# Optimization experiments

Hardware: AMD Instinct MI355X
Metric: run time of the kernel (lower is better)

## Reference

```python
import jax, jax.numpy as jnp
import numpy as np

L, D, DH, NH, P = 12, 768, 64, 12, 16
B, H_IMG, W_IMG = 16, 384, 384
MAX_GRID = 64


def setup_inputs() -> dict:
    key = jax.random.key(0)
    ks = jax.random.split(key, 10)
    r = lambda k, shp: (0.02 * jax.random.normal(k, shp, dtype=jnp.float32))
    return {
        "x": jax.random.normal(ks[0], (B, 3, H_IMG, W_IMG), dtype=jnp.float32),
        "conv_w": r(ks[1], (D, 3, P, P)),
        "conv_b": jnp.zeros((D,), jnp.float32),
        "ln_w": jnp.ones((D,), jnp.float32),
        "ln_b": jnp.zeros((D,), jnp.float32),
        "pos_y_emb": r(ks[2], (MAX_GRID, D)),
        "pos_x_emb": r(ks[3], (MAX_GRID, D)),
        "mha_ln_w": jnp.ones((L, D), jnp.float32),
        "mha_ln_b": jnp.zeros((L, D), jnp.float32),
        "qw": r(ks[4], (L, D, D)),
        "kw": r(ks[5], (L, D, D)),
        "vw": r(ks[6], (L, D, D)),
        "ffn_ln_w": jnp.ones((L, D), jnp.float32),
        "ffn_ln_b": jnp.zeros((L, D), jnp.float32),
        "w1": r(ks[7], (L, D, 4 * D)),
        "b1": jnp.zeros((L, 4 * D), jnp.float32),
        "w2": r(ks[8], (L, 4 * D, D)),
        "b2": jnp.zeros((L, D), jnp.float32),
        "x_shift": 0,
        "y_shift": 0,
    }


def _ln(x, w, b):
    m = jnp.mean(x, axis=-1, keepdims=True)
    v = jnp.var(x, axis=-1, keepdims=True)
    return (x - m) * jax.lax.rsqrt(v + 1e-5) * w + b


def reference(x, conv_w, conv_b, ln_w, ln_b, pos_y_emb, pos_x_emb,
              mha_ln_w, mha_ln_b, qw, kw, vw,
              ffn_ln_w, ffn_ln_b, w1, b1, w2, b2, x_shift, y_shift):
    # patch embed: conv + relu, to NHWC, layernorm
    h = jax.lax.conv_general_dilated(x, conv_w, (P, P), 'VALID',
                                     dimension_numbers=('NCHW', 'OIHW', 'NCHW'))
    h = jax.nn.relu(h + conv_b[None, :, None, None])
    h = jnp.transpose(h, (0, 2, 3, 1))  # [B, GH, GW, D]
    h = _ln(h, ln_w, ln_b)
    b, gh, gw, d = h.shape
    n = gh * gw
    # 2D factorized positional embedding, shared layernorm
    pos = (pos_y_emb[jnp.arange(gh) + y_shift][:, None, :]
           + pos_x_emb[jnp.arange(gw) + x_shift][None, :, :])  # [GH, GW, D]
    pos = _ln(pos, ln_w, ln_b).reshape(1, n, d)
    pos_emb = jnp.broadcast_to(pos, (b, n, d))
    t = h.reshape(b, n, d) + pos_emb
    scale = 1.0 / jnp.sqrt(jnp.float32(DH))
    for i in range(L):
        # pre-LN MHA (no output projection, mask=None / pretrain=False)
        tl = _ln(t, mha_ln_w[i], mha_ln_b[i])
        q = (tl @ qw[i]).reshape(b, n, NH, DH).transpose(0, 2, 1, 3)
        k = (tl @ kw[i]).reshape(b, n, NH, DH).transpose(0, 2, 1, 3)
        v = (tl @ vw[i]).reshape(b, n, NH, DH).transpose(0, 2, 1, 3)
        attn = jax.nn.softmax(jnp.einsum('bhqd,bhkd->bhqk', q, k) * scale, axis=-1)
        o = jnp.einsum('bhqk,bhkd->bhqd', attn, v).transpose(0, 2, 1, 3).reshape(b, n, d)
        t = t + o
        fl = _ln(t, ffn_ln_w[i], ffn_ln_b[i])
        t = t + (jax.nn.relu(fl @ w1[i] + b1[i]) @ w2[i] + b2[i])
    return t, pos_emb
```

## Files before the change

kernel.cpp:

```cpp
#include <hip/hip_runtime.h>

typedef unsigned short u16;
typedef __attribute__((ext_vector_type(4))) float f32x4;
typedef __attribute__((ext_vector_type(8))) short s16x8;

__device__ __forceinline__ u16 f2bf(float f) {
    union { float f; unsigned u; } v; v.f = f;
    unsigned r = v.u + 0x7FFFu + ((v.u >> 16) & 1u);
    return (u16)(r >> 16);
}

__device__ __forceinline__ void gload_lds16(const u16* g, u16* l) {
    __builtin_amdgcn_global_load_lds(
        (const __attribute__((address_space(1))) unsigned int*)(g),
        (__attribute__((address_space(3))) unsigned int*)(l),
        16, 0, 0);
}

#define NTOK 9216
#define SEQ  576
#define DMODEL 768
#define DFF  3072
#define NHEAD 12
#define HDIM 64

__global__ __launch_bounds__(256) void convert_bf16_kernel(const float* __restrict__ in,
                                                           u16* __restrict__ out, int n) {
    for (int i = blockIdx.x * 256 + threadIdx.x; i < n; i += gridDim.x * 256)
        out[i] = f2bf(in[i]);
}

__global__ __launch_bounds__(256) void copy_f32_kernel(const float* __restrict__ in,
                                                       float* __restrict__ out, int n4) {
    const float4* a = (const float4*)in;
    float4* o = (float4*)out;
    for (int i = blockIdx.x * 256 + threadIdx.x; i < n4; i += gridDim.x * 256)
        o[i] = a[i];
}

__global__ __launch_bounds__(256) void im2col_kernel(const float* __restrict__ x,
                                                     u16* __restrict__ out) {
    int tok = blockIdx.x;
    int b = tok / SEQ, n = tok % SEQ;
    int gy = n / 24, gx = n % 24;
    int tid = threadIdx.x;
#pragma unroll
    for (int j = 0; j < 3; ++j) {
        int col = tid + j * 256;
        int c = col >> 8, py = (col >> 4) & 15, px = col & 15;
        float v = x[(size_t)((b * 3 + c) * 384 + gy * 16 + py) * 384 + gx * 16 + px];
        out[(size_t)tok * DMODEL + col] = f2bf(v);
    }
}

__global__ __launch_bounds__(256) void transpose_layer_kernel(
        const float* __restrict__ qw, const float* __restrict__ kw, const float* __restrict__ vw,
        const float* __restrict__ w1, const float* __restrict__ w2,
        u16* __restrict__ wTq, u16* __restrict__ wTk, u16* __restrict__ wTv,
        u16* __restrict__ w1T, u16* __restrict__ w2T) {
    int bid = blockIdx.x;
    const float* src; u16* dst; int Kd, Nd, tile;
    if (bid < 1728)      { int m = bid / 576; src = m == 0 ? qw : (m == 1 ? kw : vw);
                           dst = m == 0 ? wTq : (m == 1 ? wTk : wTv); Kd = 768; Nd = 768; tile = bid % 576; }
    else if (bid < 4032) { src = w1; dst = w1T; Kd = 768; Nd = 3072; tile = bid - 1728; }
    else                 { src = w2; dst = w2T; Kd = 3072; Nd = 768; tile = bid - 4032; }
    int ntx = Nd / 32;
    int tk = (tile / ntx) * 32, tn = (tile % ntx) * 32;
    __shared__ float ts[32][33];
    int tx = threadIdx.x & 31, ty = threadIdx.x >> 5;
#pragma unroll
    for (int j = 0; j < 32; j += 8)
        ts[ty + j][tx] = src[(size_t)(tk + ty + j) * Nd + tn + tx];
    __syncthreads();
#pragma unroll
    for (int j = 0; j < 32; j += 8)
        dst[(size_t)(tn + ty + j) * Kd + tk + tx] = f2bf(ts[tx][ty + j]);
}

__global__ __launch_bounds__(256) void ln_bf16_kernel(const float* __restrict__ X,
                                                      const float* __restrict__ w,
                                                      const float* __restrict__ b,
                                                      u16* __restrict__ Y) {
    int row = blockIdx.x, tid = threadIdx.x;
    const float* x = X + (size_t)row * DMODEL;
    float v0 = x[tid], v1 = x[tid + 256], v2 = x[tid + 512];
    float s = v0 + v1 + v2, sq = v0 * v0 + v1 * v1 + v2 * v2;
#pragma unroll
    for (int off = 32; off >= 1; off >>= 1) { s += __shfl_down(s, off); sq += __shfl_down(sq, off); }
    __shared__ float red[8];
    if ((tid & 63) == 0) { red[tid >> 6] = s; red[4 + (tid >> 6)] = sq; }
    __syncthreads();
    float S = red[0] + red[1] + red[2] + red[3];
    float Q = red[4] + red[5] + red[6] + red[7];
    float mean = S * (1.f / DMODEL);
    float var = Q * (1.f / DMODEL) - mean * mean;
    float inv = rsqrtf(var + 1e-5f);
    u16* y = Y + (size_t)row * DMODEL;
    y[tid]       = f2bf((v0 - mean) * inv * w[tid]       + b[tid]);
    y[tid + 256] = f2bf((v1 - mean) * inv * w[tid + 256] + b[tid + 256]);
    y[tid + 512] = f2bf((v2 - mean) * inv * w[tid + 512] + b[tid + 512]);
}

__global__ __launch_bounds__(256) void ln_add_pos_kernel(float* __restrict__ T,
                                                         const float* __restrict__ w,
                                                         const float* __restrict__ b,
                                                         const float* __restrict__ posln) {
    int row = blockIdx.x, tid = threadIdx.x;
    float* x = T + (size_t)row * DMODEL;
    const float* p = posln + (size_t)(row % SEQ) * DMODEL;
    float v0 = x[tid], v1 = x[tid + 256], v2 = x[tid + 512];
    float s = v0 + v1 + v2, sq = v0 * v0 + v1 * v1 + v2 * v2;
#pragma unroll
    for (int off = 32; off >= 1; off >>= 1) { s += __shfl_down(s, off); sq += __shfl_down(sq, off); }
    __shared__ float red[8];
    if ((tid & 63) == 0) { red[tid >> 6] = s; red[4 + (tid >> 6)] = sq; }
    __syncthreads();
    float S = red[0] + red[1] + red[2] + red[3];
    float Q = red[4] + red[5] + red[6] + red[7];
    float mean = S * (1.f / DMODEL);
    float var = Q * (1.f / DMODEL) - mean * mean;
    float inv = rsqrtf(var + 1e-5f);
    x[tid]       = (v0 - mean) * inv * w[tid]       + b[tid]       + p[tid];
    x[tid + 256] = (v1 - mean) * inv * w[tid + 256] + b[tid + 256] + p[tid + 256];
    x[tid + 512] = (v2 - mean) * inv * w[tid + 512] + b[tid + 512] + p[tid + 512];
}

__global__ __launch_bounds__(256) void pos_ln_kernel(const float* __restrict__ py,
                                                     const float* __restrict__ px,
                                                     const float* __restrict__ w,
                                                     const float* __restrict__ b,
                                                     const int* __restrict__ xs_p,
                                                     const int* __restrict__ ys_p,
                                                     float* __restrict__ posln,
                                                     float* __restrict__ out2) {
    int row = blockIdx.x;
    int gy = row / 24, gx = row % 24;
    int ys = ys_p[0], xs = xs_p[0];
    int tid = threadIdx.x;
    float v[3]; float s = 0.f, sq = 0.f;
#pragma unroll
    for (int j = 0; j < 3; ++j) {
        int c = tid + j * 256;
        v[j] = py[(size_t)(gy + ys) * DMODEL + c] + px[(size_t)(gx + xs) * DMODEL + c];
        s += v[j]; sq += v[j] * v[j];
    }
#pragma unroll
    for (int off = 32; off >= 1; off >>= 1) { s += __shfl_down(s, off); sq += __shfl_down(sq, off); }
    __shared__ float red[8];
    if ((tid & 63) == 0) { red[tid >> 6] = s; red[4 + (tid >> 6)] = sq; }
    __syncthreads();
    float S = red[0] + red[1] + red[2] + red[3];
    float Q = red[4] + red[5] + red[6] + red[7];
    float mean = S * (1.f / DMODEL);
    float var = Q * (1.f / DMODEL) - mean * mean;
    float inv = rsqrtf(var + 1e-5f);
#pragma unroll
    for (int j = 0; j < 3; ++j) {
        int c = tid + j * 256;
        float y = (v[j] - mean) * inv * w[c] + b[c];
        posln[(size_t)row * DMODEL + c] = y;
        for (int bb = 0; bb < 16; ++bb)
            out2[((size_t)bb * SEQ + row) * DMODEL + c] = y;
    }
}

#define EPI_CONV 0
#define EPI_QKV  1
#define EPI_FFN1 3
#define EPI_FFN2 4

template <int EPI>
__global__ __launch_bounds__(512, 2) void gemm3(const u16* __restrict__ A,
                                                const u16* __restrict__ Bt,
                                                float* __restrict__ outF,
                                                u16* __restrict__ outB,
                                                u16* __restrict__ outB2,
                                                u16* __restrict__ outB3,
                                                const float* __restrict__ bias,
                                                int M, int N, int K) {
    __shared__ __align__(16) u16 lds[3 * 24576];
    const int tid = threadIdx.x;
    const int wave = tid >> 6, lane = tid & 63;
    const int c_lo = lane & 15, c_hi = lane >> 4;
    const int wm = wave >> 2, wn = wave & 3;
    const int m0 = blockIdx.x * 128, n0 = blockIdx.y * 256;

    int rowA[2], kkA[2], rowB[4], kkB[4];
#pragma unroll
    for (int r = 0; r < 2; ++r) {
        int L = r * 8192 + tid * 16;
        int P = L ^ ((L >> 3) & 0x70);
        rowA[r] = P >> 7; kkA[r] = (P & 127) >> 1;
    }
#pragma unroll
    for (int r = 0; r < 4; ++r) {
        int L = r * 8192 + tid * 16;
        int P = L ^ ((L >> 3) & 0x70);
        rowB[r] = P >> 7; kkB[r] = (P & 127) >> 1;
    }
    const int NT = K >> 6;
    f32x4 acc[4][4] = {};

    auto stage = [&](int t) {
        u16* buf = lds + (t % 3) * 24576;
        int k0 = t << 6;
#pragma unroll
        for (int r = 0; r < 2; ++r)
            gload_lds16(A + (size_t)(m0 + rowA[r]) * K + k0 + kkA[r],
                        buf + r * 4096 + wave * 512);
#pragma unroll
        for (int r = 0; r < 4; ++r)
            gload_lds16(Bt + (size_t)(n0 + rowB[r]) * K + k0 + kkB[r],
                        buf + 8192 + r * 4096 + wave * 512);
    };

    stage(0); stage(1);
    asm volatile("s_waitcnt vmcnt(6)" ::: "memory");
    __builtin_amdgcn_s_barrier();
    __builtin_amdgcn_sched_barrier(0);

    for (int t = 0; t < NT; ++t) {
        if (t + 2 < NT) stage(t + 2);
        const u16* Ab = lds + (t % 3) * 24576;
        const u16* Bb = Ab + 8192;
        s16x8 af[4][2], bf[4][2];
#pragma unroll
        for (int mf = 0; mf < 4; ++mf)
#pragma unroll
            for (int ks = 0; ks < 2; ++ks) {
                int by = (wm * 64 + mf * 16 + c_lo) * 128 + (ks * 32 + c_hi * 8) * 2;
                by ^= (by >> 3) & 0x70;
                af[mf][ks] = *(const s16x8*)((const char*)Ab + by);
            }
#pragma unroll
        for (int nf = 0; nf < 4; ++nf)
#pragma unroll
            for (int ks = 0; ks < 2; ++ks) {
                int by = (wn * 64 + nf * 16 + c_lo) * 128 + (ks * 32 + c_hi * 8) * 2;
                by ^= (by >> 3) & 0x70;
                bf[nf][ks] = *(const s16x8*)((const char*)Bb + by);
            }
        __builtin_amdgcn_s_setprio(1);
#pragma unroll
        for (int mf = 0; mf < 4; ++mf)
#pragma unroll
            for (int nf = 0; nf < 4; ++nf)
#pragma unroll
                for (int ks = 0; ks < 2; ++ks)
                    acc[mf][nf] = __builtin_amdgcn_mfma_f32_16x16x32_bf16(
                        af[mf][ks], bf[nf][ks], acc[mf][nf], 0, 0, 0);
        __builtin_amdgcn_s_setprio(0);
        if (t + 2 < NT) { asm volatile("s_waitcnt vmcnt(6)" ::: "memory"); }
        else            { asm volatile("s_waitcnt vmcnt(0)" ::: "memory"); }
        __builtin_amdgcn_s_barrier();
        __builtin_amdgcn_sched_barrier(0);
    }

#pragma unroll
    for (int mf = 0; mf < 4; ++mf)
#pragma unroll
        for (int nf = 0; nf < 4; ++nf)
#pragma unroll
            for (int r = 0; r < 4; ++r) {
                int grow = m0 + wm * 64 + mf * 16 + c_hi * 4 + r;
                int gcol = n0 + wn * 64 + nf * 16 + c_lo;
                float v = acc[mf][nf][r];
                if (EPI == EPI_CONV) {
                    v += bias[gcol]; v = fmaxf(v, 0.f);
                    outF[(size_t)grow * N + gcol] = v;
                } else if (EPI == EPI_QKV) {
                    int sel = n0 / 768;
                    int lcol = gcol - sel * 768;
                    if (sel == 0)      outB [(size_t)grow * 768 + lcol] = f2bf(v);
                    else if (sel == 1) outB2[(size_t)grow * 768 + lcol] = f2bf(v);
                    else {
                        int b = grow / SEQ, nt = grow % SEQ;
                        int h = lcol >> 6, dh = lcol & 63;
                        outB3[(size_t)(((b * NHEAD + h) << 6) + dh) * SEQ + nt] = f2bf(v);
                    }
                } else if (EPI == EPI_FFN1) {
                    v += bias[gcol]; v = fmaxf(v, 0.f);
                    outB[(size_t)grow * N + gcol] = f2bf(v);
                } else if (EPI == EPI_FFN2) {
                    outF[(size_t)grow * DMODEL + gcol] += v + bias[gcol];
                }
            }
}

__global__ __launch_bounds__(256) void attn_kernel(const u16* __restrict__ Qb,
                                                   const u16* __restrict__ Kb,
                                                   const u16* __restrict__ Vt,
                                                   float* __restrict__ T) {
    int bid = blockIdx.x;
    int qt = bid % 9, h = (bid / 9) % NHEAD, b = bid / (9 * NHEAD);
    int q0 = qt * 64;
    const int tid = threadIdx.x, wave = tid >> 6, lane = tid & 63;
    const int c_lo = lane & 15, c_hi = lane >> 4;
    __shared__ __align__(16) u16 Qs[64][72];
    __shared__ __align__(16) u16 Ks[64][72];
    __shared__ __align__(16) u16 Vs[64][72];
    __shared__ __align__(16) u16 Ps[4][16][72];
#pragma unroll
    for (int i = 0; i < 2; ++i) {
        int c = i * 256 + tid, row = c >> 3, slot = (c & 7) * 8;
        *(s16x8*)&Qs[row][slot] =
            *(const s16x8*)(Qb + ((size_t)(b * SEQ + q0 + row) * DMODEL + h * HDIM + slot));
    }
    f32x4 o[4] = {};
    float mrun[4], lrun[4];
#pragma unroll
    for (int r = 0; r < 4; ++r) { mrun[r] = -1e30f; lrun[r] = 0.f; }
    for (int t2 = 0; t2 < 9; ++t2) {
        int kv0 = t2 * 64;
        __syncthreads();
#pragma unroll
        for (int i = 0; i < 2; ++i) {
            int c = i * 256 + tid, row = c >> 3, slot = (c & 7) * 8;
            *(s16x8*)&Ks[row][slot] =
                *(const s16x8*)(Kb + ((size_t)(b * SEQ + kv0 + row) * DMODEL + h * HDIM + slot));
            *(s16x8*)&Vs[row][slot] =
                *(const s16x8*)(Vt + ((size_t)((b * NHEAD + h) * HDIM + row) * SEQ + kv0 + slot));
        }
        __syncthreads();
        f32x4 s[4] = {};
        s16x8 aq[2];
#pragma unroll
        for (int ks = 0; ks < 2; ++ks)
            aq[ks] = *(const s16x8*)&Qs[wave * 16 + c_lo][ks * 32 + c_hi * 8];
#pragma unroll
        for (int nf = 0; nf < 4; ++nf)
#pragma unroll
            for (int ks = 0; ks < 2; ++ks) {
                s16x8 bk = *(const s16x8*)&Ks[nf * 16 + c_lo][ks * 32 + c_hi * 8];
                s[nf] = __builtin_amdgcn_mfma_f32_16x16x32_bf16(aq[ks], bk, s[nf], 0, 0, 0);
            }
#pragma unroll
        for (int nf = 0; nf < 4; ++nf)
#pragma unroll
            for (int r = 0; r < 4; ++r) s[nf][r] *= 0.125f;
        float mx[4];
#pragma unroll
        for (int r = 0; r < 4; ++r)
            mx[r] = fmaxf(fmaxf(s[0][r], s[1][r]), fmaxf(s[2][r], s[3][r]));
#pragma unroll
        for (int off = 1; off < 16; off <<= 1)
#pragma unroll
            for (int r = 0; r < 4; ++r) mx[r] = fmaxf(mx[r], __shfl_xor(mx[r], off));
        float alpha[4];
#pragma unroll
        for (int r = 0; r < 4; ++r) {
            float mn = fmaxf(mrun[r], mx[r]);
            alpha[r] = __expf(mrun[r] - mn);
            mrun[r] = mn;
            lrun[r] *= alpha[r];
        }
        float ls[4] = {0.f, 0.f, 0.f, 0.f};
        u16 pb[4][4];
#pragma unroll
        for (int nf = 0; nf < 4; ++nf)
#pragma unroll
            for (int r = 0; r < 4; ++r) {
                float p = __expf(s[nf][r] - mrun[r]);
                ls[r] += p;
                pb[nf][r] = f2bf(p);
            }
#pragma unroll
        for (int off = 1; off < 16; off <<= 1)
#pragma unroll
            for (int r = 0; r < 4; ++r) ls[r] += __shfl_xor(ls[r], off);
#pragma unroll
        for (int r = 0; r < 4; ++r) lrun[r] += ls[r];
#pragma unroll
        for (int df = 0; df < 4; ++df)
#pragma unroll
            for (int r = 0; r < 4; ++r) o[df][r] *= alpha[r];
#pragma unroll
        for (int nf = 0; nf < 4; ++nf)
#pragma unroll
            for (int r = 0; r < 4; ++r)
                Ps[wave][c_hi * 4 + r][c_lo + nf * 16] = pb[nf][r];
        asm volatile("s_waitcnt lgkmcnt(0)" ::: "memory");
        s16x8 pa[2];
#pragma unroll
        for (int ks = 0; ks < 2; ++ks)
            pa[ks] = *(const s16x8*)&Ps[wave][c_lo][ks * 32 + c_hi * 8];
#pragma unroll
        for (int df = 0; df < 4; ++df)
#pragma unroll
            for (int ks = 0; ks < 2; ++ks) {
                s16x8 bv = *(const s16x8*)&Vs[df * 16 + c_lo][ks * 32 + c_hi * 8];
                o[df] = __builtin_amdgcn_mfma_f32_16x16x32_bf16(pa[ks], bv, o[df], 0, 0, 0);
            }
    }
#pragma unroll
    for (int df = 0; df < 4; ++df)
#pragma unroll
        for (int r = 0; r < 4; ++r) {
            int grow = b * SEQ + q0 + wave * 16 + c_hi * 4 + r;
            int gcol = h * HDIM + df * 16 + c_lo;
            T[(size_t)grow * DMODEL + gcol] += o[df][r] / lrun[r];
        }
}

extern "C" void kernel_launch(void* const* d_in, const int* in_sizes, int n_in,
                              void* d_out, int out_size, void* d_ws, size_t ws_size,
                              hipStream_t stream) {
    (void)in_sizes; (void)n_in; (void)out_size; (void)ws_size;
    const float* x        = (const float*)d_in[0];
    const float* conv_w   = (const float*)d_in[1];
    const float* conv_b   = (const float*)d_in[2];
    const float* ln_w     = (const float*)d_in[3];
    const float* ln_b     = (const float*)d_in[4];
    const float* pos_y    = (const float*)d_in[5];
    const float* pos_x    = (const float*)d_in[6];
    const float* mha_ln_w = (const float*)d_in[7];
    const float* mha_ln_b = (const float*)d_in[8];
    const float* qw       = (const float*)d_in[9];
    const float* kw       = (const float*)d_in[10];
    const float* vw       = (const float*)d_in[11];
    const float* ffn_ln_w = (const float*)d_in[12];
    const float* ffn_ln_b = (const float*)d_in[13];
    const float* w1       = (const float*)d_in[14];
    const float* b1       = (const float*)d_in[15];
    const float* w2       = (const float*)d_in[16];
    const float* b2       = (const float*)d_in[17];
    const int*   xs       = (const int*)d_in[18];
    const int*   ys       = (const int*)d_in[19];
    float* out1 = (float*)d_out;
    float* out2 = out1 + (size_t)NTOK * DMODEL;

    size_t off = 0;
    char* ws = (char*)d_ws;
    auto carve = [&](size_t bytes) { char* p = ws + off; off += (bytes + 255) & ~(size_t)255; return p; };
    u16* wTqkv = (u16*)carve((size_t)3 * 768 * 768 * 2);
    u16* w1T = (u16*)carve((size_t)DFF * DMODEL * 2);
    u16* w2T = (u16*)carve((size_t)DMODEL * DFF * 2);
    float* t  = (float*)carve((size_t)NTOK * DMODEL * 4);
    u16* tl   = (u16*)carve((size_t)NTOK * DMODEL * 2);
    u16* qb   = (u16*)carve((size_t)NTOK * DMODEL * 2);
    u16* kb   = (u16*)carve((size_t)NTOK * DMODEL * 2);
    u16* vT   = (u16*)carve((size_t)NTOK * DMODEL * 2);
    u16* hb   = (u16*)carve((size_t)NTOK * DFF * 2);
    float* posln = (float*)carve((size_t)SEQ * DMODEL * 4);
    u16* wTq = wTqkv;
    u16* wTk = wTqkv + (size_t)768 * 768;
    u16* wTv = wTqkv + (size_t)2 * 768 * 768;
    u16* cw   = wTqkv;
    u16* im2c = hb;

    convert_bf16_kernel<<<1152, 256, 0, stream>>>(conv_w, cw, 768 * 768);
    im2col_kernel<<<NTOK, 256, 0, stream>>>(x, im2c);
    gemm3<EPI_CONV><<<dim3(72, 3), 512, 0, stream>>>(im2c, cw, t, nullptr, nullptr, nullptr,
                                                     conv_b, NTOK, DMODEL, DMODEL);
    pos_ln_kernel<<<SEQ, 256, 0, stream>>>(pos_y, pos_x, ln_w, ln_b, xs, ys, posln, out2);
    ln_add_pos_kernel<<<NTOK, 256, 0, stream>>>(t, ln_w, ln_b, posln);

    for (int i = 0; i < 12; ++i) {
        transpose_layer_kernel<<<6336, 256, 0, stream>>>(
            qw + (size_t)i * 768 * 768, kw + (size_t)i * 768 * 768, vw + (size_t)i * 768 * 768,
            w1 + (size_t)i * 768 * DFF, w2 + (size_t)i * DFF * 768,
            wTq, wTk, wTv, w1T, w2T);
        ln_bf16_kernel<<<NTOK, 256, 0, stream>>>(t, mha_ln_w + i * DMODEL, mha_ln_b + i * DMODEL, tl);
        gemm3<EPI_QKV><<<dim3(72, 9), 512, 0, stream>>>(tl, wTqkv, nullptr, qb, kb, vT,
                                                        nullptr, NTOK, 3 * DMODEL, DMODEL);
        attn_kernel<<<16 * NHEAD * 9, 256, 0, stream>>>(qb, kb, vT, t);
        ln_bf16_kernel<<<NTOK, 256, 0, stream>>>(t, ffn_ln_w + i * DMODEL, ffn_ln_b + i * DMODEL, tl);
        gemm3<EPI_FFN1><<<dim3(72, 12), 512, 0, stream>>>(tl, w1T, nullptr, hb, nullptr, nullptr,
                                                          b1 + (size_t)i * DFF, NTOK, DFF, DMODEL);
        gemm3<EPI_FFN2><<<dim3(72, 3), 512, 0, stream>>>(hb, w2T, t, nullptr, nullptr, nullptr,
                                                         b2 + (size_t)i * DMODEL, NTOK, DMODEL, DFF);
    }
    copy_f32_kernel<<<2048, 256, 0, stream>>>(t, out1, (NTOK * DMODEL) / 4);
}
```

Before: 3.256 ms.

## Use 256x256 double-buffered GEMM for QKV/FFN1 and register-prefetch K/V in attention

```diff
diff --git a/kernel.cpp b/kernel.cpp
--- a/kernel.cpp
+++ b/kernel.cpp
@@ -170,7 +170,7 @@
 #define EPI_FFN2 4
 
 template <int EPI>
-__global__ __launch_bounds__(512, 2) void gemm3(const u16* __restrict__ A,
+__global__ __launch_bounds__(512, 2) void gemm8(const u16* __restrict__ A,
                                                 const u16* __restrict__ Bt,
                                                 float* __restrict__ outF,
                                                 u16* __restrict__ outB,
@@ -178,97 +178,96 @@
                                                 u16* __restrict__ outB3,
                                                 const float* __restrict__ bias,
                                                 int M, int N, int K) {
-    __shared__ __align__(16) u16 lds[3 * 24576];
+    __shared__ __align__(16) u16 lds[2 * 32768];
     const int tid = threadIdx.x;
     const int wave = tid >> 6, lane = tid & 63;
     const int c_lo = lane & 15, c_hi = lane >> 4;
     const int wm = wave >> 2, wn = wave & 3;
-    const int m0 = blockIdx.x * 128, n0 = blockIdx.y * 256;
-
-    int rowA[2], kkA[2], rowB[4], kkB[4];
-#pragma unroll
-    for (int r = 0; r < 2; ++r) {
-        int L = r * 8192 + tid * 16;
-        int P = L ^ ((L >> 3) & 0x70);
-        rowA[r] = P >> 7; kkA[r] = (P & 127) >> 1;
-    }
+    const int m0 = blockIdx.x * 256, n0 = blockIdx.y * 256;
+
+    const u16* srcA[4]; const u16* srcB[4]; int dA[4], dB[4];
 #pragma unroll
     for (int r = 0; r < 4; ++r) {
         int L = r * 8192 + tid * 16;
         int P = L ^ ((L >> 3) & 0x70);
-        rowB[r] = P >> 7; kkB[r] = (P & 127) >> 1;
+        srcA[r] = A  + (size_t)(m0 + (P >> 7)) * K + ((P & 127) >> 1);
+        srcB[r] = Bt + (size_t)(n0 + (P >> 7)) * K + ((P & 127) >> 1);
+        dA[r] = r * 4096 + tid * 8;
+        dB[r] = 16384 + r * 4096 + tid * 8;
     }
     const int NT = K >> 6;
-    f32x4 acc[4][4] = {};
+    f32x4 acc[8][4] = {};
 
     auto stage = [&](int t) {
-        u16* buf = lds + (t % 3) * 24576;
-        int k0 = t << 6;
-#pragma unroll
-        for (int r = 0; r < 2; ++r)
-            gload_lds16(A + (size_t)(m0 + rowA[r]) * K + k0 + kkA[r],
-                        buf + r * 4096 + wave * 512);
-#pragma unroll
-        for (int r = 0; r < 4; ++r)
-            gload_lds16(Bt + (size_t)(n0 + rowB[r]) * K + k0 + kkB[r],
-                        buf + 8192 + r * 4096 + wave * 512);
+        u16* buf = lds + (t & 1) * 32768;
+        int ko = t << 6;
+#pragma unroll
+        for (int r = 0; r < 4; ++r) {
+            gload_lds16(srcA[r] + ko, buf + dA[r]);
+            gload_lds16(srcB[r] + ko, buf + dB[r]);
+        }
     };
 
-    stage(0); stage(1);
-    asm volatile("s_waitcnt vmcnt(6)" ::: "memory");
+    stage(0);
+    asm volatile("s_waitcnt vmcnt(0)" ::: "memory");
     __builtin_amdgcn_s_barrier();
     __builtin_amdgcn_sched_barrier(0);
 
     for (int t = 0; t < NT; ++t) {
-        if (t + 2 < NT) stage(t + 2);
-        const u16* Ab = lds + (t % 3) * 24576;
-        const u16* Bb = Ab + 8192;
-        s16x8 af[4][2], bf[4][2];
-#pragma unroll
-        for (int mf = 0; mf < 4; ++mf)
-#pragma unroll
-            for (int ks = 0; ks < 2; ++ks) {
-                int by = (wm * 64 + mf * 16 + c_lo) * 128 + (ks * 32 + c_hi * 8) * 2;
-                by ^= (by >> 3) & 0x70;
-                af[mf][ks] = *(const s16x8*)((const char*)Ab + by);
-            }
-#pragma unroll
-        for (int nf = 0; nf < 4; ++nf)
-#pragma unroll
-            for (int ks = 0; ks < 2; ++ks) {
-                int by = (wn * 64 + nf * 16 + c_lo) * 128 + (ks * 32 + c_hi * 8) * 2;
-                by ^= (by >> 3) & 0x70;
-                bf[nf][ks] = *(const s16x8*)((const char*)Bb + by);
-            }
-        __builtin_amdgcn_s_setprio(1);
-#pragma unroll
-        for (int mf = 0; mf < 4; ++mf)
-#pragma unroll
-            for (int nf = 0; nf < 4; ++nf)
-#pragma unroll
-                for (int ks = 0; ks < 2; ++ks)
-                    acc[mf][nf] = __builtin_amdgcn_mfma_f32_16x16x32_bf16(
-                        af[mf][ks], bf[nf][ks], acc[mf][nf], 0, 0, 0);
-        __builtin_amdgcn_s_setprio(0);
-        if (t + 2 < NT) { asm volatile("s_waitcnt vmcnt(6)" ::: "memory"); }
-        else            { asm volatile("s_waitcnt vmcnt(0)" ::: "memory"); }
-        __builtin_amdgcn_s_barrier();
+        if (t + 1 < NT) stage(t + 1);
         __builtin_amdgcn_sched_barrier(0);
-    }
-
-#pragma unroll
-    for (int mf = 0; mf < 4; ++mf)
+        const char* Ab = (const char*)(lds + (t & 1) * 32768);
+        const char* Bb = Ab + 32768;
+#pragma unroll
+        for (int p = 0; p < 4; ++p) {
+            const int mh = p >> 1, nh = p & 1;
+            s16x8 af[4][2], bf[2][2];
+#pragma unroll
+            for (int i = 0; i < 4; ++i)
+#pragma unroll
+                for (int ks = 0; ks < 2; ++ks) {
+                    int by = (wm * 128 + (mh * 4 + i) * 16 + c_lo) * 128 + (ks * 32 + c_hi * 8) * 2;
+                    by ^= (by >> 3) & 0x70;
+                    af[i][ks] = *(const s16x8*)(Ab + by);
+                }
+#pragma unroll
+            for (int j = 0; j < 2; ++j)
+#pragma unroll
+                for (int ks = 0; ks < 2; ++ks) {
+                    int by = (wn * 64 + (nh * 2 + j) * 16 + c_lo) * 128 + (ks * 32 + c_hi * 8) * 2;
+                    by ^= (by >> 3) & 0x70;
+                    bf[j][ks] = *(const s16x8*)(Bb + by);
+                }
+            asm volatile("s_waitcnt lgkmcnt(0)" ::: "memory");
+            __builtin_amdgcn_sched_barrier(0);
+            __builtin_amdgcn_s_setprio(1);
+#pragma unroll
+            for (int i = 0; i < 4; ++i)
+#pragma unroll
+                for (int j = 0; j < 2; ++j)
+#pragma unroll
+                    for (int ks = 0; ks < 2; ++ks)
+                        acc[mh * 4 + i][nh * 2 + j] = __builtin_amdgcn_mfma_f32_16x16x32_bf16(
+                            af[i][ks], bf[j][ks], acc[mh * 4 + i][nh * 2 + j], 0, 0, 0);
+            __builtin_amdgcn_s_setprio(0);
+        }
+        if (t + 1 < NT) {
+            asm volatile("s_waitcnt vmcnt(0)" ::: "memory");
+            __builtin_amdgcn_s_barrier();
+            __builtin_amdgcn_sched_barrier(0);
+        }
+    }
+
+#pragma unroll
+    for (int mf = 0; mf < 8; ++mf)
 #pragma unroll
         for (int nf = 0; nf < 4; ++nf)
 #pragma unroll
             for (int r = 0; r < 4; ++r) {
-                int grow = m0 + wm * 64 + mf * 16 + c_hi * 4 + r;
+                int grow = m0 + wm * 128 + mf * 16 + c_hi * 4 + r;
                 int gcol = n0 + wn * 64 + nf * 16 + c_lo;
                 float v = acc[mf][nf][r];
-                if (EPI == EPI_CONV) {
-                    v += bias[gcol]; v = fmaxf(v, 0.f);
-                    outF[(size_t)grow * N + gcol] = v;
-                } else if (EPI == EPI_QKV) {
+                if (EPI == EPI_QKV) {
                     int sel = n0 / 768;
                     int lcol = gcol - sel * 768;
                     if (sel == 0)      outB [(size_t)grow * 768 + lcol] = f2bf(v);
@@ -281,6 +280,109 @@
                 } else if (EPI == EPI_FFN1) {
                     v += bias[gcol]; v = fmaxf(v, 0.f);
                     outB[(size_t)grow * N + gcol] = f2bf(v);
+                }
+            }
+}
+
+template <int EPI>
+__global__ __launch_bounds__(512, 2) void gemm3(const u16* __restrict__ A,
+                                                const u16* __restrict__ Bt,
+                                                float* __restrict__ outF,
+                                                u16* __restrict__ outB,
+                                                const float* __restrict__ bias,
+                                                int M, int N, int K) {
+    __shared__ __align__(16) u16 lds[3 * 24576];
+    const int tid = threadIdx.x;
+    const int wave = tid >> 6, lane = tid & 63;
+    const int c_lo = lane & 15, c_hi = lane >> 4;
+    const int wm = wave >> 2, wn = wave & 3;
+    const int m0 = blockIdx.x * 128, n0 = blockIdx.y * 256;
+
+    int rowA[2], kkA[2], rowB[4], kkB[4];
+#pragma unroll
+    for (int r = 0; r < 2; ++r) {
+        int L = r * 8192 + tid * 16;
+        int P = L ^ ((L >> 3) & 0x70);
+        rowA[r] = P >> 7; kkA[r] = (P & 127) >> 1;
+    }
+#pragma unroll
+    for (int r = 0; r < 4; ++r) {
+        int L = r * 8192 + tid * 16;
+        int P = L ^ ((L >> 3) & 0x70);
+        rowB[r] = P >> 7; kkB[r] = (P & 127) >> 1;
+    }
+    const int NT = K >> 6;
+    f32x4 acc[4][4] = {};
+
+    auto stage = [&](int t) {
+        u16* buf = lds + (t % 3) * 24576;
+        int k0 = t << 6;
+#pragma unroll
+        for (int r = 0; r < 2; ++r)
+            gload_lds16(A + (size_t)(m0 + rowA[r]) * K + k0 + kkA[r],
+                        buf + r * 4096 + wave * 512);
+#pragma unroll
+        for (int r = 0; r < 4; ++r)
+            gload_lds16(Bt + (size_t)(n0 + rowB[r]) * K + k0 + kkB[r],
+                        buf + 8192 + r * 4096 + wave * 512);
+    };
+
+    stage(0); stage(1);
+    asm volatile("s_waitcnt vmcnt(6)" ::: "memory");
+    __builtin_amdgcn_s_barrier();
+    __builtin_amdgcn_sched_barrier(0);
+
+    for (int t = 0; t < NT; ++t) {
+        if (t + 2 < NT) stage(t + 2);
+        const u16* Ab = lds + (t % 3) * 24576;
+        const u16* Bb = Ab + 8192;
+        s16x8 af[4][2], bf[4][2];
+#pragma unroll
+        for (int mf = 0; mf < 4; ++mf)
+#pragma unroll
+            for (int ks = 0; ks < 2; ++ks) {
+                int by = (wm * 64 + mf * 16 + c_lo) * 128 + (ks * 32 + c_hi * 8) * 2;
+                by ^= (by >> 3) & 0x70;
+                af[mf][ks] = *(const s16x8*)((const char*)Ab + by);
+            }
+#pragma unroll
+        for (int nf = 0; nf < 4; ++nf)
+#pragma unroll
+            for (int ks = 0; ks < 2; ++ks) {
+                int by = (wn * 64 + nf * 16 + c_lo) * 128 + (ks * 32 + c_hi * 8) * 2;
+                by ^= (by >> 3) & 0x70;
+                bf[nf][ks] = *(const s16x8*)((const char*)Bb + by);
+            }
+        asm volatile("s_waitcnt lgkmcnt(0)" ::: "memory");
+        __builtin_amdgcn_sched_barrier(0);
+        __builtin_amdgcn_s_setprio(1);
+#pragma unroll
+        for (int mf = 0; mf < 4; ++mf)
+#pragma unroll
+            for (int nf = 0; nf < 4; ++nf)
+#pragma unroll
+                for (int ks = 0; ks < 2; ++ks)
+                    acc[mf][nf] = __builtin_amdgcn_mfma_f32_16x16x32_bf16(
+                        af[mf][ks], bf[nf][ks], acc[mf][nf], 0, 0, 0);
+        __builtin_amdgcn_s_setprio(0);
+        if (t + 2 < NT) { asm volatile("s_waitcnt vmcnt(6)" ::: "memory"); }
+        else            { asm volatile("s_waitcnt vmcnt(0)" ::: "memory"); }
+        __builtin_amdgcn_s_barrier();
+        __builtin_amdgcn_sched_barrier(0);
+    }
+
+#pragma unroll
+    for (int mf = 0; mf < 4; ++mf)
+#pragma unroll
+        for (int nf = 0; nf < 4; ++nf)
+#pragma unroll
+            for (int r = 0; r < 4; ++r) {
+                int grow = m0 + wm * 64 + mf * 16 + c_hi * 4 + r;
+                int gcol = n0 + wn * 64 + nf * 16 + c_lo;
+                float v = acc[mf][nf][r];
+                if (EPI == EPI_CONV) {
+                    v += bias[gcol]; v = fmaxf(v, 0.f);
+                    outF[(size_t)grow * N + gcol] = v;
                 } else if (EPI == EPI_FFN2) {
                     outF[(size_t)grow * DMODEL + gcol] += v + bias[gcol];
                 }
@@ -292,7 +394,8 @@
                                                    const u16* __restrict__ Vt,
                                                    float* __restrict__ T) {
     int bid = blockIdx.x;
-    int qt = bid % 9, h = (bid / 9) % NHEAD, b = bid / (9 * NHEAD);
+    int qt = bid / 192, bh = bid % 192;
+    int b = bh / NHEAD, h = bh % NHEAD;
     int q0 = qt * 64;
     const int tid = threadIdx.x, wave = tid >> 6, lane = tid & 63;
     const int c_lo = lane & 15, c_hi = lane >> 4;
@@ -306,22 +409,39 @@
         *(s16x8*)&Qs[row][slot] =
             *(const s16x8*)(Qb + ((size_t)(b * SEQ + q0 + row) * DMODEL + h * HDIM + slot));
     }
+    s16x8 kreg[2], vreg[2];
+    {
+#pragma unroll
+        for (int i = 0; i < 2; ++i) {
+            int c = i * 256 + tid, row = c >> 3, slot = (c & 7) * 8;
+            kreg[i] = *(const s16x8*)(Kb + ((size_t)(b * SEQ + row) * DMODEL + h * HDIM + slot));
+            vreg[i] = *(const s16x8*)(Vt + ((size_t)((b * NHEAD + h) * HDIM + row) * SEQ + slot));
+        }
+    }
     f32x4 o[4] = {};
     float mrun[4], lrun[4];
 #pragma unroll
     for (int r = 0; r < 4; ++r) { mrun[r] = -1e30f; lrun[r] = 0.f; }
     for (int t2 = 0; t2 < 9; ++t2) {
-        int kv0 = t2 * 64;
-        __syncthreads();
+        __builtin_amdgcn_s_barrier();
 #pragma unroll
         for (int i = 0; i < 2; ++i) {
             int c = i * 256 + tid, row = c >> 3, slot = (c & 7) * 8;
-            *(s16x8*)&Ks[row][slot] =
-                *(const s16x8*)(Kb + ((size_t)(b * SEQ + kv0 + row) * DMODEL + h * HDIM + slot));
-            *(s16x8*)&Vs[row][slot] =
-                *(const s16x8*)(Vt + ((size_t)((b * NHEAD + h) * HDIM + row) * SEQ + kv0 + slot));
-        }
-        __syncthreads();
+            *(s16x8*)&Ks[row][slot] = kreg[i];
+            *(s16x8*)&Vs[row][slot] = vreg[i];
+        }
+        asm volatile("s_waitcnt lgkmcnt(0)" ::: "memory");
+        __builtin_amdgcn_s_barrier();
+        __builtin_amdgcn_sched_barrier(0);
+        if (t2 < 8) {
+            int kv0 = (t2 + 1) * 64;
+#pragma unroll
+            for (int i = 0; i < 2; ++i) {
+                int c = i * 256 + tid, row = c >> 3, slot = (c & 7) * 8;
+                kreg[i] = *(const s16x8*)(Kb + ((size_t)(b * SEQ + kv0 + row) * DMODEL + h * HDIM + slot));
+                vreg[i] = *(const s16x8*)(Vt + ((size_t)((b * NHEAD + h) * HDIM + row) * SEQ + kv0 + slot));
+            }
+        }
         f32x4 s[4] = {};
         s16x8 aq[2];
 #pragma unroll
@@ -450,7 +570,7 @@
 
     convert_bf16_kernel<<<1152, 256, 0, stream>>>(conv_w, cw, 768 * 768);
     im2col_kernel<<<NTOK, 256, 0, stream>>>(x, im2c);
-    gemm3<EPI_CONV><<<dim3(72, 3), 512, 0, stream>>>(im2c, cw, t, nullptr, nullptr, nullptr,
+    gemm3<EPI_CONV><<<dim3(72, 3), 512, 0, stream>>>(im2c, cw, t, nullptr,
                                                      conv_b, NTOK, DMODEL, DMODEL);
     pos_ln_kernel<<<SEQ, 256, 0, stream>>>(pos_y, pos_x, ln_w, ln_b, xs, ys, posln, out2);
     ln_add_pos_kernel<<<NTOK, 256, 0, stream>>>(t, ln_w, ln_b, posln);
@@ -461,13 +581,13 @@
             w1 + (size_t)i * 768 * DFF, w2 + (size_t)i * DFF * 768,
             wTq, wTk, wTv, w1T, w2T);
         ln_bf16_kernel<<<NTOK, 256, 0, stream>>>(t, mha_ln_w + i * DMODEL, mha_ln_b + i * DMODEL, tl);
-        gemm3<EPI_QKV><<<dim3(72, 9), 512, 0, stream>>>(tl, wTqkv, nullptr, qb, kb, vT,
+        gemm8<EPI_QKV><<<dim3(36, 9), 512, 0, stream>>>(tl, wTqkv, nullptr, qb, kb, vT,
                                                         nullptr, NTOK, 3 * DMODEL, DMODEL);
         attn_kernel<<<16 * NHEAD * 9, 256, 0, stream>>>(qb, kb, vT, t);
         ln_bf16_kernel<<<NTOK, 256, 0, stream>>>(t, ffn_ln_w + i * DMODEL, ffn_ln_b + i * DMODEL, tl);
-        gemm3<EPI_FFN1><<<dim3(72, 12), 512, 0, stream>>>(tl, w1T, nullptr, hb, nullptr, nullptr,
+        gemm8<EPI_FFN1><<<dim3(36, 12), 512, 0, stream>>>(tl, w1T, nullptr, hb, nullptr, nullptr,
                                                           b1 + (size_t)i * DFF, NTOK, DFF, DMODEL);
-        gemm3<EPI_FFN2><<<dim3(72, 3), 512, 0, stream>>>(hb, w2T, t, nullptr, nullptr, nullptr,
+        gemm3<EPI_FFN2><<<dim3(72, 3), 512, 0, stream>>>(hb, w2T, t, nullptr,
                                                          b2 + (size_t)i * DMODEL, NTOK, DMODEL, DFF);
     }
     copy_f32_kernel<<<2048, 256, 0, stream>>>(t, out1, (NTOK * DMODEL) / 4);
```

Result: slower. 3.403 ms (+4.5%).

## Replace GEMM with 256x256 tiles, XCD-aware remap, split-K FFN2 and prefetched attention

Applied to the files above, without the earlier changes.

```diff
diff --git a/kernel.cpp b/kernel.cpp
--- a/kernel.cpp
+++ b/kernel.cpp
@@ -169,105 +169,110 @@
 #define EPI_FFN1 3
 #define EPI_FFN2 4
 
-template <int EPI>
-__global__ __launch_bounds__(512, 2) void gemm3(const u16* __restrict__ A,
-                                                const u16* __restrict__ Bt,
-                                                float* __restrict__ outF,
-                                                u16* __restrict__ outB,
-                                                u16* __restrict__ outB2,
-                                                u16* __restrict__ outB3,
-                                                const float* __restrict__ bias,
-                                                int M, int N, int K) {
-    __shared__ __align__(16) u16 lds[3 * 24576];
+template <int EPI, int NKT>
+__global__ __launch_bounds__(512, 2) void gemm256(const u16* __restrict__ A,
+                                                  const u16* __restrict__ Bt,
+                                                  float* __restrict__ outF,
+                                                  u16* __restrict__ outB,
+                                                  u16* __restrict__ outB2,
+                                                  u16* __restrict__ outB3,
+                                                  const float* __restrict__ bias,
+                                                  int lda, int N, int NBY) {
+    __shared__ __align__(16) u16 lds[4 * 16384];
     const int tid = threadIdx.x;
     const int wave = tid >> 6, lane = tid & 63;
     const int c_lo = lane & 15, c_hi = lane >> 4;
     const int wm = wave >> 2, wn = wave & 3;
-    const int m0 = blockIdx.x * 128, n0 = blockIdx.y * 256;
-
-    int rowA[2], kkA[2], rowB[4], kkB[4];
-#pragma unroll
-    for (int r = 0; r < 2; ++r) {
-        int L = r * 8192 + tid * 16;
-        int P = L ^ ((L >> 3) & 0x70);
-        rowA[r] = P >> 7; kkA[r] = (P & 127) >> 1;
-    }
-#pragma unroll
-    for (int r = 0; r < 4; ++r) {
-        int L = r * 8192 + tid * 16;
-        int P = L ^ ((L >> 3) & 0x70);
-        rowB[r] = P >> 7; kkB[r] = (P & 127) >> 1;
-    }
-    const int NT = K >> 6;
-    f32x4 acc[4][4] = {};
-
-    auto stage = [&](int t) {
-        u16* buf = lds + (t % 3) * 24576;
-        int k0 = t << 6;
-#pragma unroll
-        for (int r = 0; r < 2; ++r)
-            gload_lds16(A + (size_t)(m0 + rowA[r]) * K + k0 + kkA[r],
-                        buf + r * 4096 + wave * 512);
-#pragma unroll
-        for (int r = 0; r < 4; ++r)
-            gload_lds16(Bt + (size_t)(n0 + rowB[r]) * K + k0 + kkB[r],
-                        buf + 8192 + r * 4096 + wave * 512);
+    int nwg = gridDim.x, bid = blockIdx.x;
+    int xcd = bid & 7, loc = bid >> 3;
+    int q = nwg >> 3, r = nwg & 7;
+    int lid = (xcd < r ? xcd * (q + 1) : r * (q + 1) + (xcd - r) * q) + loc;
+    int bx = lid % 36, rest = lid / 36;
+    int by = rest % NBY, bz = rest / NBY;
+    const int m0 = bx * 256, n0 = by * 256;
+    const int kb = bz * NKT * 32;
+
+    const u16* sA = A  + (size_t)(m0 + (tid >> 2)) * lda + kb + (tid & 3) * 8;
+    const u16* sB = Bt + (size_t)(n0 + (tid >> 2)) * lda + kb + (tid & 3) * 8;
+    const size_t rstep = (size_t)128 * lda;
+    f32x4 acc[8][4] = {};
+
+    auto stageA = [&](int kt) {
+        u16* d = lds + (kt & 3) * 16384 + tid * 8;
+        gload_lds16(sA + kt * 32, d);
+        gload_lds16(sA + rstep + kt * 32, d + 4096);
     };
-
-    stage(0); stage(1);
-    asm volatile("s_waitcnt vmcnt(6)" ::: "memory");
+    auto stageB = [&](int kt) {
+        u16* d = lds + (kt & 3) * 16384 + 8192 + tid * 8;
+        gload_lds16(sB + kt * 32, d);
+        gload_lds16(sB + rstep + kt * 32, d + 4096);
+    };
+
+    stageA(0); stageB(0); stageA(1); stageB(1); stageA(2); stageB(2);
+    asm volatile("s_waitcnt vmcnt(8)" ::: "memory");
     __builtin_amdgcn_s_barrier();
     __builtin_amdgcn_sched_barrier(0);
 
-    for (int t = 0; t < NT; ++t) {
-        if (t + 2 < NT) stage(t + 2);
-        const u16* Ab = lds + (t % 3) * 24576;
-        const u16* Bb = Ab + 8192;
-        s16x8 af[4][2], bf[4][2];
-#pragma unroll
-        for (int mf = 0; mf < 4; ++mf)
-#pragma unroll
-            for (int ks = 0; ks < 2; ++ks) {
-                int by = (wm * 64 + mf * 16 + c_lo) * 128 + (ks * 32 + c_hi * 8) * 2;
-                by ^= (by >> 3) & 0x70;
-                af[mf][ks] = *(const s16x8*)((const char*)Ab + by);
-            }
+    for (int j = 0; j < NKT; ++j) {
+        const u16* buf = lds + (j & 3) * 16384;
+        const bool st = (j + 3 < NKT);
+        s16x8 af[4], bf[4];
+#pragma unroll
+        for (int i = 0; i < 4; ++i) {
+            int row = wm * 128 + i * 16 + c_lo;
+            af[i] = *(const s16x8*)(buf + row * 32 + c_hi * 8);
+        }
+#pragma unroll
+        for (int n = 0; n < 4; ++n) {
+            int row = wn * 64 + n * 16 + c_lo;
+            bf[n] = *(const s16x8*)(buf + 8192 + row * 32 + c_hi * 8);
+        }
+        if (st) stageA(j + 3);
+        __builtin_amdgcn_s_barrier();
+        asm volatile("s_waitcnt lgkmcnt(0)" ::: "memory");
+        __builtin_amdgcn_sched_barrier(0);
+        __builtin_amdgcn_s_setprio(1);
+#pragma unroll
+        for (int i = 0; i < 4; ++i)
+#pragma unroll
+            for (int n = 0; n < 4; ++n)
+                acc[i][n] = __builtin_amdgcn_mfma_f32_16x16x32_bf16(af[i], bf[n], acc[i][n], 0, 0, 0);
+        __builtin_amdgcn_s_setprio(0);
+        __builtin_amdgcn_s_barrier();
+#pragma unroll
+        for (int i = 0; i < 4; ++i) {
+            int row = wm * 128 + 64 + i * 16 + c_lo;
+            af[i] = *(const s16x8*)(buf + row * 32 + c_hi * 8);
+        }
+        if (st) stageB(j + 3);
+        __builtin_amdgcn_s_barrier();
+        asm volatile("s_waitcnt lgkmcnt(0)" ::: "memory");
+        __builtin_amdgcn_sched_barrier(0);
+        __builtin_amdgcn_s_setprio(1);
+#pragma unroll
+        for (int i = 0; i < 4; ++i)
+#pragma unroll
+            for (int n = 0; n < 4; ++n)
+                acc[4 + i][n] = __builtin_amdgcn_mfma_f32_16x16x32_bf16(af[i], bf[n], acc[4 + i][n], 0, 0, 0);
+        __builtin_amdgcn_s_setprio(0);
+        if (j <= NKT - 4)      { asm volatile("s_waitcnt vmcnt(8)" ::: "memory"); }
+        else if (j < NKT - 1)  { asm volatile("s_waitcnt vmcnt(0)" ::: "memory"); }
+        __builtin_amdgcn_s_barrier();
+        __builtin_amdgcn_sched_barrier(0);
+    }
+
+#pragma unroll
+    for (int mf = 0; mf < 8; ++mf)
 #pragma unroll
         for (int nf = 0; nf < 4; ++nf)
 #pragma unroll
-            for (int ks = 0; ks < 2; ++ks) {
-                int by = (wn * 64 + nf * 16 + c_lo) * 128 + (ks * 32 + c_hi * 8) * 2;
-                by ^= (by >> 3) & 0x70;
-                bf[nf][ks] = *(const s16x8*)((const char*)Bb + by);
-            }
-        __builtin_amdgcn_s_setprio(1);
-#pragma unroll
-        for (int mf = 0; mf < 4; ++mf)
-#pragma unroll
-            for (int nf = 0; nf < 4; ++nf)
-#pragma unroll
-                for (int ks = 0; ks < 2; ++ks)
-                    acc[mf][nf] = __builtin_amdgcn_mfma_f32_16x16x32_bf16(
-                        af[mf][ks], bf[nf][ks], acc[mf][nf], 0, 0, 0);
-        __builtin_amdgcn_s_setprio(0);
-        if (t + 2 < NT) { asm volatile("s_waitcnt vmcnt(6)" ::: "memory"); }
-        else            { asm volatile("s_waitcnt vmcnt(0)" ::: "memory"); }
-        __builtin_amdgcn_s_barrier();
-        __builtin_amdgcn_sched_barrier(0);
-    }
-
-#pragma unroll
-    for (int mf = 0; mf < 4; ++mf)
-#pragma unroll
-        for (int nf = 0; nf < 4; ++nf)
-#pragma unroll
-            for (int r = 0; r < 4; ++r) {
-                int grow = m0 + wm * 64 + mf * 16 + c_hi * 4 + r;
+            for (int rr = 0; rr < 4; ++rr) {
+                int grow = m0 + wm * 128 + mf * 16 + c_hi * 4 + rr;
                 int gcol = n0 + wn * 64 + nf * 16 + c_lo;
-                float v = acc[mf][nf][r];
+                float v = acc[mf][nf][rr];
                 if (EPI == EPI_CONV) {
                     v += bias[gcol]; v = fmaxf(v, 0.f);
-                    outF[(size_t)grow * N + gcol] = v;
+                    outF[(size_t)grow * 768 + gcol] = v;
                 } else if (EPI == EPI_QKV) {
                     int sel = n0 / 768;
                     int lcol = gcol - sel * 768;
@@ -282,7 +287,8 @@
                     v += bias[gcol]; v = fmaxf(v, 0.f);
                     outB[(size_t)grow * N + gcol] = f2bf(v);
                 } else if (EPI == EPI_FFN2) {
-                    outF[(size_t)grow * DMODEL + gcol] += v + bias[gcol];
+                    if (bz == 0) v += bias[gcol];
+                    atomicAdd(&outF[(size_t)grow * 768 + gcol], v);
                 }
             }
 }
@@ -292,7 +298,8 @@
                                                    const u16* __restrict__ Vt,
                                                    float* __restrict__ T) {
     int bid = blockIdx.x;
-    int qt = bid % 9, h = (bid / 9) % NHEAD, b = bid / (9 * NHEAD);
+    int qt = bid / 192, bh = bid % 192;
+    int b = bh / NHEAD, h = bh % NHEAD;
     int q0 = qt * 64;
     const int tid = threadIdx.x, wave = tid >> 6, lane = tid & 63;
     const int c_lo = lane & 15, c_hi = lane >> 4;
@@ -306,22 +313,39 @@
         *(s16x8*)&Qs[row][slot] =
             *(const s16x8*)(Qb + ((size_t)(b * SEQ + q0 + row) * DMODEL + h * HDIM + slot));
     }
+    s16x8 kreg[2], vreg[2];
+    {
+#pragma unroll
+        for (int i = 0; i < 2; ++i) {
+            int c = i * 256 + tid, row = c >> 3, slot = (c & 7) * 8;
+            kreg[i] = *(const s16x8*)(Kb + ((size_t)(b * SEQ + row) * DMODEL + h * HDIM + slot));
+            vreg[i] = *(const s16x8*)(Vt + ((size_t)((b * NHEAD + h) * HDIM + row) * SEQ + slot));
+        }
+    }
     f32x4 o[4] = {};
     float mrun[4], lrun[4];
 #pragma unroll
     for (int r = 0; r < 4; ++r) { mrun[r] = -1e30f; lrun[r] = 0.f; }
     for (int t2 = 0; t2 < 9; ++t2) {
-        int kv0 = t2 * 64;
-        __syncthreads();
+        __builtin_amdgcn_s_barrier();
 #pragma unroll
         for (int i = 0; i < 2; ++i) {
             int c = i * 256 + tid, row = c >> 3, slot = (c & 7) * 8;
-            *(s16x8*)&Ks[row][slot] =
-                *(const s16x8*)(Kb + ((size_t)(b * SEQ + kv0 + row) * DMODEL + h * HDIM + slot));
-            *(s16x8*)&Vs[row][slot] =
-                *(const s16x8*)(Vt + ((size_t)((b * NHEAD + h) * HDIM + row) * SEQ + kv0 + slot));
-        }
-        __syncthreads();
+            *(s16x8*)&Ks[row][slot] = kreg[i];
+            *(s16x8*)&Vs[row][slot] = vreg[i];
+        }
+        asm volatile("s_waitcnt lgkmcnt(0)" ::: "memory");
+        __builtin_amdgcn_s_barrier();
+        __builtin_amdgcn_sched_barrier(0);
+        if (t2 < 8) {
+            int kv0 = (t2 + 1) * 64;
+#pragma unroll
+            for (int i = 0; i < 2; ++i) {
+                int c = i * 256 + tid, row = c >> 3, slot = (c & 7) * 8;
+                kreg[i] = *(const s16x8*)(Kb + ((size_t)(b * SEQ + kv0 + row) * DMODEL + h * HDIM + slot));
+                vreg[i] = *(const s16x8*)(Vt + ((size_t)((b * NHEAD + h) * HDIM + row) * SEQ + kv0 + slot));
+            }
+        }
         f32x4 s[4] = {};
         s16x8 aq[2];
 #pragma unroll
@@ -450,8 +474,8 @@
 
     convert_bf16_kernel<<<1152, 256, 0, stream>>>(conv_w, cw, 768 * 768);
     im2col_kernel<<<NTOK, 256, 0, stream>>>(x, im2c);
-    gemm3<EPI_CONV><<<dim3(72, 3), 512, 0, stream>>>(im2c, cw, t, nullptr, nullptr, nullptr,
-                                                     conv_b, NTOK, DMODEL, DMODEL);
+    gemm256<EPI_CONV, 24><<<108, 512, 0, stream>>>(im2c, cw, t, nullptr, nullptr, nullptr,
+                                                   conv_b, 768, 768, 3);
     pos_ln_kernel<<<SEQ, 256, 0, stream>>>(pos_y, pos_x, ln_w, ln_b, xs, ys, posln, out2);
     ln_add_pos_kernel<<<NTOK, 256, 0, stream>>>(t, ln_w, ln_b, posln);
 
@@ -461,14 +485,14 @@
             w1 + (size_t)i * 768 * DFF, w2 + (size_t)i * DFF * 768,
             wTq, wTk, wTv, w1T, w2T);
         ln_bf16_kernel<<<NTOK, 256, 0, stream>>>(t, mha_ln_w + i * DMODEL, mha_ln_b + i * DMODEL, tl);
-        gemm3<EPI_QKV><<<dim3(72, 9), 512, 0, stream>>>(tl, wTqkv, nullptr, qb, kb, vT,
-                                                        nullptr, NTOK, 3 * DMODEL, DMODEL);
+        gemm256<EPI_QKV, 24><<<324, 512, 0, stream>>>(tl, wTqkv, nullptr, qb, kb, vT,
+                                                      nullptr, 768, 2304, 9);
         attn_kernel<<<16 * NHEAD * 9, 256, 0, stream>>>(qb, kb, vT, t);
         ln_bf16_kernel<<<NTOK, 256, 0, stream>>>(t, ffn_ln_w + i * DMODEL, ffn_ln_b + i * DMODEL, tl);
-        gemm3<EPI_FFN1><<<dim3(72, 12), 512, 0, stream>>>(tl, w1T, nullptr, hb, nullptr, nullptr,
-                                                          b1 + (size_t)i * DFF, NTOK, DFF, DMODEL);
-        gemm3<EPI_FFN2><<<dim3(72, 3), 512, 0, stream>>>(hb, w2T, t, nullptr, nullptr, nullptr,
-                                                         b2 + (size_t)i * DMODEL, NTOK, DMODEL, DFF);
+        gemm256<EPI_FFN1, 24><<<432, 512, 0, stream>>>(tl, w1T, nullptr, hb, nullptr, nullptr,
+                                                       b1 + (size_t)i * DFF, 768, 3072, 12);
+        gemm256<EPI_FFN2, 48><<<216, 512, 0, stream>>>(hb, w2T, t, nullptr, nullptr, nullptr,
+                                                       b2 + (size_t)i * DMODEL, 3072, 768, 3);
     }
     copy_f32_kernel<<<2048, 256, 0, stream>>>(t, out1, (NTOK * DMODEL) / 4);
 }
```

Result: slower. 4.476 ms (+37.5%).
